# Performance work log

Hardware: AMD Instinct MI355X
Metric: run time of the kernel (lower is better)

Reference implementation:

```python
import jax, jax.numpy as jnp
import numpy as np

B, IN, U = 4096, 256, 128
G, LW, LB = 1000, 64, 32


def setup_inputs() -> dict:
    key = jax.random.key(0)
    ks = jax.random.split(key, 9)
    return {
        "x": jax.random.normal(ks[0], (B, IN), dtype=jnp.float32),
        "eps_w": jax.random.normal(ks[1], (B, LW), dtype=jnp.float32),
        "eps_b": jax.random.normal(ks[2], (B, LB), dtype=jnp.float32),
        "zw_mu": jax.random.normal(ks[3], (G, LW), dtype=jnp.float32) * 0.05,
        "zw_sigma": jax.random.normal(ks[4], (G, LW), dtype=jnp.float32),
        "Wf": jax.random.normal(ks[5], (LW, IN * U), dtype=jnp.float32) * (1.0 / np.sqrt(LW)),
        "zb_mu": jnp.zeros((G, LB), dtype=jnp.float32),
        "zb_sigma": jax.random.normal(ks[6], (G, LB), dtype=jnp.float32),
        "Bf": jax.random.normal(ks[7], (LB, U), dtype=jnp.float32) * (1.0 / np.sqrt(LB)),
        "gid": jax.random.randint(ks[8], (B,), 0, G, dtype=jnp.int32),
    }


def reference(x, eps_w, eps_b, zw_mu, zw_sigma, Wf, zb_mu, zb_sigma, Bf, gid):
    # --- multilevel weights: gather group posterior, reparameterized sample ---
    mu_w = zw_mu[gid]                                  # [B, LW]
    sig_w = jax.nn.softplus(zw_sigma[gid])             # [B, LW]
    zw_samp = mu_w + sig_w * eps_w                     # [B, LW]
    w = (zw_samp @ Wf).reshape(B, IN, U)               # factor out to per-example weights
    # --- multilevel bias ---
    mu_b = zb_mu[gid]                                  # [B, LB]
    sig_b = jax.nn.softplus(zb_sigma[gid])             # [B, LB]
    b = (mu_b + sig_b * eps_b) @ Bf                    # [B, U]
    # --- batched per-example matmul: w^T @ x  (tf.matmul(w, x, transpose_a=True)) ---
    out = jnp.einsum("bi,biu->bu", x, w) + b           # [B, U]
    return out  # activation is None (linear)
```

## Files before the change

### kernel.cpp

```cpp
#include <hip/hip_runtime.h>
#include <hip/hip_bf16.h>
#include <stdint.h>

#define B_SZ   4096
#define IN_SZ  256
#define U_SZ   128
#define G_SZ   1000
#define LW_SZ  64
#define LB_SZ  32
#define K_SZ   (LW_SZ * IN_SZ)

#define BM     128
#define KSPL   16
#define NSTEP  16
#define NTILE  (K_SZ / 64)
#define TSH    8192

typedef __attribute__((ext_vector_type(8))) short  bf16x8;
typedef __attribute__((ext_vector_type(4))) float  f32x4;
typedef __attribute__((ext_vector_type(8))) _Float16 f16x8;
typedef __attribute__((ext_vector_type(4))) _Float16 f16x4;
typedef __attribute__((ext_vector_type(2))) _Float16 f16x2;

__device__ __forceinline__ ushort f2bf(float f) {
    unsigned u = __float_as_uint(f);
    u += 0x7fffu + ((u >> 16) & 1u);
    return (ushort)(u >> 16);
}

__device__ __forceinline__ float softplus_f(float v) {
    return fmaxf(v, 0.0f) + log1pf(__expf(-fabsf(v)));
}

__device__ __forceinline__ f16x8 mulzw(f16x8 a, f16x2 z) {
    union { f16x8 v8; f16x2 v2[4]; } in, out;
    in.v8 = a;
    #pragma unroll
    for (int w = 0; w < 4; ++w) out.v2[w] = in.v2[w] * z;
    return out.v8;
}

__global__ __launch_bounds__(256) void fmd_prep(
    const float* __restrict__ Wf, const float* __restrict__ x,
    short* __restrict__ wfT, short* __restrict__ xh)
{
    const int tid = threadIdx.x;
    if (blockIdx.x < NTILE) {
        const int bid = blockIdx.x;
        const int t = ((bid & 15) << 4) | (bid >> 4);
        __shared__ float lds[64 * 133];
        #pragma unroll
        for (int it = 0; it < 8; ++it) {
            int idx = it * 256 + tid;
            int kk = idx >> 5, u4 = idx & 31;
            float4 v = *reinterpret_cast<const float4*>(&Wf[(t * 64 + kk) * U_SZ + u4 * 4]);
            *reinterpret_cast<float4*>(&lds[kk * 133 + u4 * 4]) = v;
        }
        __syncthreads();
        short* tile = wfT + t * TSH;
        #pragma unroll
        for (int it = 0; it < 4; ++it) {
            int p = it * 256 + tid;
            int kb  = p >> 9;
            int u16 = (p >> 6) & 7;
            int l   = p & 63;
            int u   = u16 * 16 + (l & 15);
            int kk0 = kb * 32 + (l >> 4) * 8;
            union { _Float16 h[8]; f16x8 v; } pk;
            #pragma unroll
            for (int j = 0; j < 8; ++j)
                pk.h[j] = (_Float16)lds[(kk0 + j) * 133 + u];
            *reinterpret_cast<f16x8*>(&tile[p * 8]) = pk.v;
        }
    } else {
        const int bb = blockIdx.x - NTILE;
        const int mt = bb >> 2, c = bb & 3;
        short* tile = xh + bb * TSH;
        #pragma unroll
        for (int it = 0; it < 4; ++it) {
            int p = it * 256 + tid;
            int frag = p >> 6;
            int l    = p & 63;
            int wr2  = frag >> 3;
            int m2   = (frag >> 1) & 3;
            int kb   = frag & 1;
            int row  = mt * 128 + wr2 * 64 + m2 * 16 + (l & 15);
            int col  = c * 64 + kb * 32 + (l >> 4) * 8;
            const float* src = &x[row * IN_SZ + col];
            float4 a = *reinterpret_cast<const float4*>(src);
            float4 b = *reinterpret_cast<const float4*>(src + 4);
            union { _Float16 h[8]; f16x8 v; } pk;
            pk.h[0] = (_Float16)a.x; pk.h[1] = (_Float16)a.y;
            pk.h[2] = (_Float16)a.z; pk.h[3] = (_Float16)a.w;
            pk.h[4] = (_Float16)b.x; pk.h[5] = (_Float16)b.y;
            pk.h[6] = (_Float16)b.z; pk.h[7] = (_Float16)b.w;
            *reinterpret_cast<f16x8*>(&tile[p * 8]) = pk.v;
        }
    }
}

__global__ __launch_bounds__(256, 2) void fmd_gemm6(
    const short* __restrict__ xh,
    const short* __restrict__ wfT,
    const float* __restrict__ zw_mu,
    const float* __restrict__ zw_sigma,
    const float* __restrict__ eps_w,
    const int*   __restrict__ gid,
    _Float16*    __restrict__ part)
{
    const int tid  = threadIdx.x;
    const int lane = tid & 63;
    const int wid  = tid >> 6;
    const int wr   = wid >> 1;
    const int wc   = wid & 1;
    const int bid  = blockIdx.x;
    const int ks   = bid & (KSPL - 1);
    const int mt   = bid >> 4;
    const int m0   = mt * BM;
    const int lane8 = lane * 8;

    f16x2 zwp[4][4];
    #pragma unroll
    for (int m = 0; m < 4; ++m) {
        int row = wr * 64 + m * 16 + (lane & 15);
        int b   = m0 + row;
        int g   = gid[b];
        float4 mu = *reinterpret_cast<const float4*>(&zw_mu[g * LW_SZ + ks * 4]);
        float4 sg = *reinterpret_cast<const float4*>(&zw_sigma[g * LW_SZ + ks * 4]);
        float4 ep = *reinterpret_cast<const float4*>(&eps_w[b * LW_SZ + ks * 4]);
        float v0 = mu.x + softplus_f(sg.x) * ep.x;
        float v1 = mu.y + softplus_f(sg.y) * ep.y;
        float v2 = mu.z + softplus_f(sg.z) * ep.z;
        float v3 = mu.w + softplus_f(sg.w) * ep.w;
        _Float16 h0 = (_Float16)v0, h1 = (_Float16)v1, h2 = (_Float16)v2, h3 = (_Float16)v3;
        zwp[m][0] = (f16x2){h0, h0};
        zwp[m][1] = (f16x2){h1, h1};
        zwp[m][2] = (f16x2){h2, h2};
        zwp[m][3] = (f16x2){h3, h3};
    }

    f16x8 areg[2][2][4];
    f16x8 breg[2][2][4];

    {
        const short* ap = xh + (mt * 4 + 0) * TSH;
        #pragma unroll
        for (int kb = 0; kb < 2; ++kb)
            #pragma unroll
            for (int m = 0; m < 4; ++m)
                areg[0][kb][m] = *reinterpret_cast<const f16x8*>(
                    &ap[((wr * 4 + m) * 2 + kb) * 512 + lane8]);
        const short* bp = wfT + ((ks * 4 + 0) * 4 + 0) * TSH;
        #pragma unroll
        for (int kb = 0; kb < 2; ++kb)
            #pragma unroll
            for (int n = 0; n < 4; ++n)
                breg[0][kb][n] = *reinterpret_cast<const f16x8*>(
                    &bp[(kb * 8 + wc * 4 + n) * 512 + lane8]);
    }

    f32x4 acc[4][4];
    #pragma unroll
    for (int m = 0; m < 4; ++m)
        #pragma unroll
        for (int n = 0; n < 4; ++n)
            acc[m][n] = (f32x4){0.f, 0.f, 0.f, 0.f};

    #pragma unroll
    for (int c = 0; c < 4; ++c) {
        #pragma unroll
        for (int li = 0; li < 4; ++li) {
            const int s = c * 4 + li;

            if (s + 1 < NSTEP) {
                const int sn = s + 1;
                const short* bp = wfT + ((ks * 4 + (sn & 3)) * 4 + (sn >> 2)) * TSH;
                #pragma unroll
                for (int kb = 0; kb < 2; ++kb)
                    #pragma unroll
                    for (int n = 0; n < 4; ++n)
                        breg[sn & 1][kb][n] = *reinterpret_cast<const f16x8*>(
                            &bp[(kb * 8 + wc * 4 + n) * 512 + lane8]);
            }
            if (li == 2 && c < 3) {
                const short* ap = xh + (mt * 4 + c + 1) * TSH;
                #pragma unroll
                for (int kb = 0; kb < 2; ++kb)
                    #pragma unroll
                    for (int m = 0; m < 4; ++m)
                        areg[(c + 1) & 1][kb][m] = *reinterpret_cast<const f16x8*>(
                            &ap[((wr * 4 + m) * 2 + kb) * 512 + lane8]);
            }

            #pragma unroll
            for (int kb = 0; kb < 2; ++kb) {
                f16x8 as_[4];
                #pragma unroll
                for (int m = 0; m < 4; ++m)
                    as_[m] = mulzw(areg[c & 1][kb][m], zwp[m][li]);
                #pragma unroll
                for (int m = 0; m < 4; ++m)
                    #pragma unroll
                    for (int n = 0; n < 4; ++n)
                        acc[m][n] = __builtin_amdgcn_mfma_f32_16x16x32_f16(
                            as_[m], breg[s & 1][kb][n], acc[m][n], 0, 0, 0);
            }
        }
    }

    _Float16* dst = part + (size_t)ks * (B_SZ * U_SZ);
    #pragma unroll
    for (int m = 0; m < 4; ++m) {
        int row0 = m0 + wr * 64 + m * 16 + ((lane >> 4) << 2);
        #pragma unroll
        for (int n = 0; n < 4; ++n) {
            int col = wc * 64 + n * 16 + (lane & 15);
            #pragma unroll
            for (int j = 0; j < 4; ++j)
                dst[(row0 + j) * U_SZ + col] = (_Float16)acc[m][n][j];
        }
    }
}

__global__ __launch_bounds__(256) void fmd_reduce4(
    const _Float16* __restrict__ part,
    const float* __restrict__ eps_b,
    const float* __restrict__ zb_mu,
    const float* __restrict__ zb_sigma,
    const float* __restrict__ Bf,
    const int*   __restrict__ gid,
    float*       __restrict__ out)
{
    const int tid = threadIdx.x;
    const int bid = blockIdx.x;
    const int i8  = bid * 256 + tid;
    const int r   = tid >> 4;
    const int u0  = (tid & 15) * 8;

    __shared__ float zb[16][33];
    {
        int e = tid;
        int rr = e >> 5, cc = e & 31;
        int b2 = bid * 16 + rr;
        int g  = gid[b2];
        zb[rr][cc] = zb_mu[g * LB_SZ + cc]
                   + softplus_f(zb_sigma[g * LB_SZ + cc]) * eps_b[b2 * LB_SZ + cc];
        e += 256; rr = e >> 5; cc = e & 31;
        b2 = bid * 16 + rr;
        g  = gid[b2];
        zb[rr][cc] = zb_mu[g * LB_SZ + cc]
                   + softplus_f(zb_sigma[g * LB_SZ + cc]) * eps_b[b2 * LB_SZ + cc];
    }
    __syncthreads();

    f32x4 a0 = (f32x4){0.f, 0.f, 0.f, 0.f};
    f32x4 a1 = (f32x4){0.f, 0.f, 0.f, 0.f};
    #pragma unroll
    for (int l = 0; l < LB_SZ; ++l) {
        float z = zb[r][l];
        f32x4 b0 = *reinterpret_cast<const f32x4*>(&Bf[l * U_SZ + u0]);
        f32x4 b1 = *reinterpret_cast<const f32x4*>(&Bf[l * U_SZ + u0 + 4]);
        a0 += z * b0;
        a1 += z * b1;
    }

    #pragma unroll
    for (int ks = 0; ks < KSPL; ++ks) {
        f16x8 p = *reinterpret_cast<const f16x8*>(
            &part[(size_t)ks * (B_SZ * U_SZ) + (size_t)i8 * 8]);
        a0[0] += (float)p[0]; a0[1] += (float)p[1];
        a0[2] += (float)p[2]; a0[3] += (float)p[3];
        a1[0] += (float)p[4]; a1[1] += (float)p[5];
        a1[2] += (float)p[6]; a1[3] += (float)p[7];
    }
    *reinterpret_cast<f32x4*>(&out[(size_t)i8 * 8])     = a0;
    *reinterpret_cast<f32x4*>(&out[(size_t)i8 * 8 + 4]) = a1;
}

__global__ __launch_bounds__(256) void fmd_bias(
    const float* __restrict__ eps_b,
    const float* __restrict__ zb_mu,
    const float* __restrict__ zb_sigma,
    const float* __restrict__ Bf,
    const int*   __restrict__ gid,
    float*       __restrict__ out)
{
    const int half = threadIdx.x >> 7;
    const int u    = threadIdx.x & 127;
    const int b    = blockIdx.x * 2 + half;

    __shared__ float zb[2][LB_SZ];
    if (u < LB_SZ) {
        int g = gid[b];
        float sg = softplus_f(zb_sigma[g * LB_SZ + u]);
        zb[half][u] = zb_mu[g * LB_SZ + u] + sg * eps_b[b * LB_SZ + u];
    }
    __syncthreads();

    float acc = 0.0f;
    #pragma unroll
    for (int l = 0; l < LB_SZ; ++l)
        acc += zb[half][l] * Bf[l * U_SZ + u];
    out[b * U_SZ + u] = acc;
}

__global__ __launch_bounds__(256, 2) void fmd_gemm_legacy(
    const float* __restrict__ x,
    const float* __restrict__ eps_w,
    const float* __restrict__ zw_mu,
    const float* __restrict__ zw_sigma,
    const float* __restrict__ Wf,
    const int*   __restrict__ gid,
    float*       __restrict__ out)
{
    const int tid  = threadIdx.x;
    const int lane = tid & 63;
    const int wid  = tid >> 6;
    const int wr   = wid >> 1;
    const int wc   = wid & 1;
    const int bid  = blockIdx.x;
    const int ks   = bid & (KSPL - 1);
    const int mt   = bid >> 4;
    const int m0   = mt * 128;

    __shared__ short As[128 * 64];
    __shared__ short Bs[U_SZ * 64];
    __shared__ float zw_s[128][4];

    for (int it = tid; it < 128 * 4; it += 256) {
        int r = it >> 2, lloc = it & 3;
        int b = m0 + r;
        int g = gid[b];
        int l = ks * 4 + lloc;
        float sg = softplus_f(zw_sigma[g * LW_SZ + l]);
        zw_s[r][lloc] = zw_mu[g * LW_SZ + l] + sg * eps_w[b * LW_SZ + l];
    }

    f32x4 acc[4][4];
    #pragma unroll
    for (int m = 0; m < 4; ++m)
        #pragma unroll
        for (int n = 0; n < 4; ++n)
            acc[m][n] = (f32x4){0.f, 0.f, 0.f, 0.f};

    for (int s = 0; s < NSTEP; ++s) {
        __syncthreads();
        const int li = s >> 2;
        const int i0 = (s & 3) * 64;
        const int k0 = ks * (K_SZ / KSPL) + s * 64;

        #pragma unroll
        for (int it = 0; it < 8; ++it) {
            int idx = it * 256 + tid;
            int r = idx >> 4, c4 = idx & 15;
            float4 xv = *reinterpret_cast<const float4*>(&x[(m0 + r) * IN_SZ + i0 + c4 * 4]);
            float zw = zw_s[r][li];
            ushort h0 = f2bf(xv.x * zw), h1 = f2bf(xv.y * zw);
            ushort h2 = f2bf(xv.z * zw), h3 = f2bf(xv.w * zw);
            unsigned long long pw = (unsigned long long)h0
                                  | ((unsigned long long)h1 << 16)
                                  | ((unsigned long long)h2 << 32)
                                  | ((unsigned long long)h3 << 48);
            int si = (r * 64 + c4 * 4) ^ ((r & 7) << 3);
            *reinterpret_cast<unsigned long long*>(&As[si]) = pw;
        }
        #pragma unroll
        for (int it = 0; it < 4; ++it) {
            int idx = it * 256 + tid;
            int u = idx & 127, kg = idx >> 7;
            union { ushort h[8]; bf16x8 v; } pk;
            #pragma unroll
            for (int j = 0; j < 8; ++j)
                pk.h[j] = f2bf(Wf[(k0 + kg * 8 + j) * U_SZ + u]);
            int si = (u * 64 + kg * 8) ^ ((u & 7) << 3);
            *reinterpret_cast<bf16x8*>(&Bs[si]) = pk.v;
        }
        __syncthreads();

        #pragma unroll
        for (int kb = 0; kb < 2; ++kb) {
            bf16x8 af[4], bfr[4];
            #pragma unroll
            for (int m = 0; m < 4; ++m) {
                int row = wr * 64 + m * 16 + (lane & 15);
                int si = (row * 64 + kb * 32 + (lane >> 4) * 8) ^ ((row & 7) << 3);
                af[m] = *reinterpret_cast<const bf16x8*>(&As[si]);
            }
            #pragma unroll
            for (int n = 0; n < 4; ++n) {
                int rowu = wc * 64 + n * 16 + (lane & 15);
                int si = (rowu * 64 + kb * 32 + (lane >> 4) * 8) ^ ((rowu & 7) << 3);
                bfr[n] = *reinterpret_cast<const bf16x8*>(&Bs[si]);
            }
            #pragma unroll
            for (int m = 0; m < 4; ++m)
                #pragma unroll
                for (int n = 0; n < 4; ++n)
                    acc[m][n] = __builtin_amdgcn_mfma_f32_16x16x32_bf16(af[m], bfr[n], acc[m][n], 0, 0, 0);
        }
    }

    #pragma unroll
    for (int m = 0; m < 4; ++m) {
        int row0 = m0 + wr * 64 + m * 16 + ((lane >> 4) << 2);
        #pragma unroll
        for (int n = 0; n < 4; ++n) {
            int col = wc * 64 + n * 16 + (lane & 15);
            #pragma unroll
            for (int j = 0; j < 4; ++j)
                atomicAdd(&out[(row0 + j) * U_SZ + col], acc[m][n][j]);
        }
    }
}

extern "C" void kernel_launch(void* const* d_in, const int* in_sizes, int n_in,
                              void* d_out, int out_size, void* d_ws, size_t ws_size,
                              hipStream_t stream) {
    const float* x        = (const float*)d_in[0];
    const float* eps_w    = (const float*)d_in[1];
    const float* eps_b    = (const float*)d_in[2];
    const float* zw_mu    = (const float*)d_in[3];
    const float* zw_sigma = (const float*)d_in[4];
    const float* Wf       = (const float*)d_in[5];
    const float* zb_mu    = (const float*)d_in[6];
    const float* zb_sigma = (const float*)d_in[7];
    const float* Bf       = (const float*)d_in[8];
    const int*   gid      = (const int*)d_in[9];
    float* out = (float*)d_out;

    const size_t WFT_BYTES  = (size_t)K_SZ * U_SZ * 2;
    const size_t XH_OFF     = WFT_BYTES;
    const size_t XH_BYTES   = (size_t)B_SZ * IN_SZ * 2;
    const size_t PART_OFF   = XH_OFF + XH_BYTES;
    const size_t PART_BYTES = (size_t)KSPL * B_SZ * U_SZ * 2;

    if (ws_size >= PART_OFF + PART_BYTES) {
        short*     wfT  = (short*)d_ws;
        short*     xh   = (short*)((char*)d_ws + XH_OFF);
        _Float16*  part = (_Float16*)((char*)d_ws + PART_OFF);
        fmd_prep<<<NTILE + (B_SZ / BM) * 4, 256, 0, stream>>>(Wf, x, wfT, xh);
        fmd_gemm6<<<(B_SZ / BM) * KSPL, 256, 0, stream>>>(
            xh, wfT, zw_mu, zw_sigma, eps_w, gid, part);
        fmd_reduce4<<<(B_SZ * U_SZ) / 2048, 256, 0, stream>>>(
            part, eps_b, zb_mu, zb_sigma, Bf, gid, out);
    } else {
        fmd_bias<<<B_SZ / 2, 256, 0, stream>>>(eps_b, zb_mu, zb_sigma, Bf, gid, out);
        fmd_gemm_legacy<<<(B_SZ / 128) * KSPL, 256, 0, stream>>>(
            x, eps_w, zw_mu, zw_sigma, Wf, gid, out);
    }
}
```

Measured before the change: 43.28 us.

## Stage GEMM tiles through swizzled LDS with direct global-to-LDS loads

Replaces the register-direct fragment loading in the split-K GEMM with double-buffered LDS staging filled by global_load_lds. The M tile grows to 256 rows with 512-thread blocks. The prep kernel now writes XOR-swizzled row-major tiles of x and the transposed Wf so LDS reads avoid bank conflicts. The aim is to raise reuse of each loaded tile across more waves and to cut global-load register pressure, at the cost of a block-wide barrier every step and only one block per CU.

```diff
diff --git a/kernel.cpp b/kernel.cpp
--- a/kernel.cpp
+++ b/kernel.cpp
@@ -10,17 +10,21 @@
 #define LB_SZ  32
 #define K_SZ   (LW_SZ * IN_SZ)
 
-#define BM     128
+#define BM     256
+#define BK     64
 #define KSPL   16
 #define NSTEP  16
-#define NTILE  (K_SZ / 64)
-#define TSH    8192
+#define NTILE  (K_SZ / BK)
+#define BCHUNK 8192
+#define ACHUNK 16384
 
 typedef __attribute__((ext_vector_type(8))) short  bf16x8;
 typedef __attribute__((ext_vector_type(4))) float  f32x4;
 typedef __attribute__((ext_vector_type(8))) _Float16 f16x8;
-typedef __attribute__((ext_vector_type(4))) _Float16 f16x4;
 typedef __attribute__((ext_vector_type(2))) _Float16 f16x2;
+
+typedef const void __attribute__((address_space(1)))* gas_ptr;
+typedef void __attribute__((address_space(3)))* las_ptr;
 
 __device__ __forceinline__ ushort f2bf(float f) {
     unsigned u = __float_as_uint(f);
@@ -57,49 +61,44 @@
             *reinterpret_cast<float4*>(&lds[kk * 133 + u4 * 4]) = v;
         }
         __syncthreads();
-        short* tile = wfT + t * TSH;
-        #pragma unroll
-        for (int it = 0; it < 4; ++it) {
-            int p = it * 256 + tid;
-            int kb  = p >> 9;
-            int u16 = (p >> 6) & 7;
-            int l   = p & 63;
-            int u   = u16 * 16 + (l & 15);
-            int kk0 = kb * 32 + (l >> 4) * 8;
+        short* tile = wfT + t * BCHUNK;
+        #pragma unroll
+        for (int g = 0; g < 4; ++g) {
+            int p = g * 2048 + tid * 8;
+            int u = p >> 6;
+            int cc = p & 63;
+            int kk0 = cc ^ ((u & 7) << 3);
             union { _Float16 h[8]; f16x8 v; } pk;
             #pragma unroll
             for (int j = 0; j < 8; ++j)
                 pk.h[j] = (_Float16)lds[(kk0 + j) * 133 + u];
-            *reinterpret_cast<f16x8*>(&tile[p * 8]) = pk.v;
+            *reinterpret_cast<f16x8*>(&tile[p]) = pk.v;
         }
     } else {
-        const int bb = blockIdx.x - NTILE;
+        const int e  = blockIdx.x - NTILE;
+        const int bb = e >> 1, h = e & 1;
         const int mt = bb >> 2, c = bb & 3;
-        short* tile = xh + bb * TSH;
+        short* chunk = xh + bb * ACHUNK;
         #pragma unroll
         for (int it = 0; it < 4; ++it) {
-            int p = it * 256 + tid;
-            int frag = p >> 6;
-            int l    = p & 63;
-            int wr2  = frag >> 3;
-            int m2   = (frag >> 1) & 3;
-            int kb   = frag & 1;
-            int row  = mt * 128 + wr2 * 64 + m2 * 16 + (l & 15);
-            int col  = c * 64 + kb * 32 + (l >> 4) * 8;
-            const float* src = &x[row * IN_SZ + col];
+            int q = h * 1024 + it * 256 + tid;
+            int r  = q >> 3;
+            int c0 = (q & 7) * 8;
+            int cc0 = c0 ^ ((r & 7) << 3);
+            const float* src = &x[(mt * BM + r) * IN_SZ + c * 64 + cc0];
             float4 a = *reinterpret_cast<const float4*>(src);
             float4 b = *reinterpret_cast<const float4*>(src + 4);
-            union { _Float16 h[8]; f16x8 v; } pk;
-            pk.h[0] = (_Float16)a.x; pk.h[1] = (_Float16)a.y;
-            pk.h[2] = (_Float16)a.z; pk.h[3] = (_Float16)a.w;
-            pk.h[4] = (_Float16)b.x; pk.h[5] = (_Float16)b.y;
-            pk.h[6] = (_Float16)b.z; pk.h[7] = (_Float16)b.w;
-            *reinterpret_cast<f16x8*>(&tile[p * 8]) = pk.v;
-        }
-    }
-}
-
-__global__ __launch_bounds__(256, 2) void fmd_gemm6(
+            union { _Float16 hh[8]; f16x8 v; } pk;
+            pk.hh[0] = (_Float16)a.x; pk.hh[1] = (_Float16)a.y;
+            pk.hh[2] = (_Float16)a.z; pk.hh[3] = (_Float16)a.w;
+            pk.hh[4] = (_Float16)b.x; pk.hh[5] = (_Float16)b.y;
+            pk.hh[6] = (_Float16)b.z; pk.hh[7] = (_Float16)b.w;
+            *reinterpret_cast<f16x8*>(&chunk[q * 8]) = pk.v;
+        }
+    }
+}
+
+__global__ __launch_bounds__(512, 1) void fmd_gemm8(
     const short* __restrict__ xh,
     const short* __restrict__ wfT,
     const float* __restrict__ zw_mu,
@@ -117,7 +116,9 @@
     const int ks   = bid & (KSPL - 1);
     const int mt   = bid >> 4;
     const int m0   = mt * BM;
-    const int lane8 = lane * 8;
+
+    __shared__ short As[2][ACHUNK];
+    __shared__ short Bs[2][BCHUNK];
 
     f16x2 zwp[4][4];
     #pragma unroll
@@ -128,36 +129,31 @@
         float4 mu = *reinterpret_cast<const float4*>(&zw_mu[g * LW_SZ + ks * 4]);
         float4 sg = *reinterpret_cast<const float4*>(&zw_sigma[g * LW_SZ + ks * 4]);
         float4 ep = *reinterpret_cast<const float4*>(&eps_w[b * LW_SZ + ks * 4]);
-        float v0 = mu.x + softplus_f(sg.x) * ep.x;
-        float v1 = mu.y + softplus_f(sg.y) * ep.y;
-        float v2 = mu.z + softplus_f(sg.z) * ep.z;
-        float v3 = mu.w + softplus_f(sg.w) * ep.w;
-        _Float16 h0 = (_Float16)v0, h1 = (_Float16)v1, h2 = (_Float16)v2, h3 = (_Float16)v3;
+        _Float16 h0 = (_Float16)(mu.x + softplus_f(sg.x) * ep.x);
+        _Float16 h1 = (_Float16)(mu.y + softplus_f(sg.y) * ep.y);
+        _Float16 h2 = (_Float16)(mu.z + softplus_f(sg.z) * ep.z);
+        _Float16 h3 = (_Float16)(mu.w + softplus_f(sg.w) * ep.w);
         zwp[m][0] = (f16x2){h0, h0};
         zwp[m][1] = (f16x2){h1, h1};
         zwp[m][2] = (f16x2){h2, h2};
         zwp[m][3] = (f16x2){h3, h3};
     }
 
-    f16x8 areg[2][2][4];
-    f16x8 breg[2][2][4];
+    const int so = tid * 8;
 
     {
-        const short* ap = xh + (mt * 4 + 0) * TSH;
-        #pragma unroll
-        for (int kb = 0; kb < 2; ++kb)
-            #pragma unroll
-            for (int m = 0; m < 4; ++m)
-                areg[0][kb][m] = *reinterpret_cast<const f16x8*>(
-                    &ap[((wr * 4 + m) * 2 + kb) * 512 + lane8]);
-        const short* bp = wfT + ((ks * 4 + 0) * 4 + 0) * TSH;
-        #pragma unroll
-        for (int kb = 0; kb < 2; ++kb)
-            #pragma unroll
-            for (int n = 0; n < 4; ++n)
-                breg[0][kb][n] = *reinterpret_cast<const f16x8*>(
-                    &bp[(kb * 8 + wc * 4 + n) * 512 + lane8]);
-    }
+        const short* sB = wfT + ((ks * 4 + 0) * 4 + 0) * BCHUNK;
+        #pragma unroll
+        for (int j = 0; j < 2; ++j)
+            __builtin_amdgcn_global_load_lds((gas_ptr)(sB + j * 4096 + so),
+                                             (las_ptr)(&Bs[0][j * 4096 + so]), 16, 0, 0);
+        const short* sA = xh + (mt * 4 + 0) * ACHUNK;
+        #pragma unroll
+        for (int j = 0; j < 4; ++j)
+            __builtin_amdgcn_global_load_lds((gas_ptr)(sA + j * 4096 + so),
+                                             (las_ptr)(&As[0][j * 4096 + so]), 16, 0, 0);
+    }
+    __syncthreads();
 
     f32x4 acc[4][4];
     #pragma unroll
@@ -167,45 +163,58 @@
             acc[m][n] = (f32x4){0.f, 0.f, 0.f, 0.f};
 
     #pragma unroll
-    for (int c = 0; c < 4; ++c) {
-        #pragma unroll
-        for (int li = 0; li < 4; ++li) {
-            const int s = c * 4 + li;
-
-            if (s + 1 < NSTEP) {
-                const int sn = s + 1;
-                const short* bp = wfT + ((ks * 4 + (sn & 3)) * 4 + (sn >> 2)) * TSH;
+    for (int s = 0; s < NSTEP; ++s) {
+        const int c  = s >> 2;
+        const int li = s & 3;
+
+        if (s + 1 < NSTEP) {
+            const int sn = s + 1;
+            const short* sB = wfT + ((ks * 4 + (sn & 3)) * 4 + (sn >> 2)) * BCHUNK;
+            short* dB = &Bs[sn & 1][0];
+            #pragma unroll
+            for (int j = 0; j < 2; ++j)
+                __builtin_amdgcn_global_load_lds((gas_ptr)(sB + j * 4096 + so),
+                                                 (las_ptr)(dB + j * 4096 + so), 16, 0, 0);
+        }
+        if (li == 2 && c < 3) {
+            const short* sA = xh + (mt * 4 + c + 1) * ACHUNK;
+            short* dA = &As[(c + 1) & 1][0];
+            #pragma unroll
+            for (int j = 0; j < 4; ++j)
+                __builtin_amdgcn_global_load_lds((gas_ptr)(sA + j * 4096 + so),
+                                                 (las_ptr)(dA + j * 4096 + so), 16, 0, 0);
+        }
+        __builtin_amdgcn_sched_barrier(0);
+
+        const short* Ab = As[c & 1];
+        const short* Bb = Bs[s & 1];
+        __builtin_amdgcn_s_setprio(1);
+        #pragma unroll
+        for (int kb = 0; kb < 2; ++kb) {
+            f16x8 af[4], bfv[4];
+            #pragma unroll
+            for (int m = 0; m < 4; ++m) {
+                int row = wr * 64 + m * 16 + (lane & 15);
+                int si = (row * BK + kb * 32 + (lane >> 4) * 8) ^ ((row & 7) << 3);
+                af[m] = *reinterpret_cast<const f16x8*>(&Ab[si]);
+            }
+            #pragma unroll
+            for (int n = 0; n < 4; ++n) {
+                int rowu = wc * 64 + n * 16 + (lane & 15);
+                int si = (rowu * BK + kb * 32 + (lane >> 4) * 8) ^ ((rowu & 7) << 3);
+                bfv[n] = *reinterpret_cast<const f16x8*>(&Bb[si]);
+            }
+            #pragma unroll
+            for (int m = 0; m < 4; ++m) {
+                f16x8 as_ = mulzw(af[m], zwp[m][li]);
                 #pragma unroll
-                for (int kb = 0; kb < 2; ++kb)
-                    #pragma unroll
-                    for (int n = 0; n < 4; ++n)
-                        breg[sn & 1][kb][n] = *reinterpret_cast<const f16x8*>(
-                            &bp[(kb * 8 + wc * 4 + n) * 512 + lane8]);
+                for (int n = 0; n < 4; ++n)
+                    acc[m][n] = __builtin_amdgcn_mfma_f32_16x16x32_f16(
+                        as_, bfv[n], acc[m][n], 0, 0, 0);
             }
-            if (li == 2 && c < 3) {
-                const short* ap = xh + (mt * 4 + c + 1) * TSH;
-                #pragma unroll
-                for (int kb = 0; kb < 2; ++kb)
-                    #pragma unroll
-                    for (int m = 0; m < 4; ++m)
-                        areg[(c + 1) & 1][kb][m] = *reinterpret_cast<const f16x8*>(
-                            &ap[((wr * 4 + m) * 2 + kb) * 512 + lane8]);
-            }
-
-            #pragma unroll
-            for (int kb = 0; kb < 2; ++kb) {
-                f16x8 as_[4];
-                #pragma unroll
-                for (int m = 0; m < 4; ++m)
-                    as_[m] = mulzw(areg[c & 1][kb][m], zwp[m][li]);
-                #pragma unroll
-                for (int m = 0; m < 4; ++m)
-                    #pragma unroll
-                    for (int n = 0; n < 4; ++n)
-                        acc[m][n] = __builtin_amdgcn_mfma_f32_16x16x32_f16(
-                            as_[m], breg[s & 1][kb][n], acc[m][n], 0, 0, 0);
-            }
-        }
+        }
+        __builtin_amdgcn_s_setprio(0);
+        __syncthreads();
     }
 
     _Float16* dst = part + (size_t)ks * (B_SZ * U_SZ);
@@ -438,8 +447,8 @@
         short*     wfT  = (short*)d_ws;
         short*     xh   = (short*)((char*)d_ws + XH_OFF);
         _Float16*  part = (_Float16*)((char*)d_ws + PART_OFF);
-        fmd_prep<<<NTILE + (B_SZ / BM) * 4, 256, 0, stream>>>(Wf, x, wfT, xh);
-        fmd_gemm6<<<(B_SZ / BM) * KSPL, 256, 0, stream>>>(
+        fmd_prep<<<NTILE + 128, 256, 0, stream>>>(Wf, x, wfT, xh);
+        fmd_gemm8<<<(B_SZ / BM) * KSPL, 512, 0, stream>>>(
             xh, wfT, zw_mu, zw_sigma, eps_w, gid, part);
         fmd_reduce4<<<(B_SZ * U_SZ) / 2048, 256, 0, stream>>>(
             part, eps_b, zb_mu, zb_sigma, Bf, gid, out);
```

After: 45.32 us. 1.05x slower.
